# Performance work log

Hardware: AMD Instinct MI355X
Metric: run time of the kernel (lower is better)

## Reference

```python
import jax, jax.numpy as jnp
import numpy as np

BETA = 10.0
EPS = 1e-6


def setup_inputs() -> dict:
    key = jax.random.key(0)
    k0, k1 = jax.random.split(key)
    f0 = jax.random.normal(k0, (4, 256, 64, 64), dtype=jnp.float32)
    f1 = jax.random.normal(k1, (4, 256, 64, 64), dtype=jnp.float32)
    return {"f0": f0, "f1": f1}


def _l2norm(x, axis):
    norm = jnp.sqrt(jnp.sum(x * x, axis=axis, keepdims=True))
    return x / jnp.maximum(norm, EPS)


def reference(f0, f1):
    B, C, Ha, Wa = f0.shape
    _, _, Hb, Wb = f1.shape
    # [B, HaWa, C] and [B, HbWb, C]
    a = f0.reshape(B, C, Ha * Wa).transpose(0, 2, 1)
    b = f1.reshape(B, C, Hb * Wb).transpose(0, 2, 1)
    a = _l2norm(a, axis=2)
    b = _l2norm(b, axis=2)
    # cosine similarity scaled by beta: [B, HaWa, HbWb]
    sim = jnp.einsum('bnc,bmc->bnm', a, b) * BETA
    attn = jax.nn.softmax(sim, axis=2)
    # target coords (x, y) of image1 grid: [HbWb, 2]
    ys = jnp.arange(Hb, dtype=f0.dtype)
    xs = jnp.arange(Wb, dtype=f0.dtype)
    yy, xx = jnp.meshgrid(ys, xs, indexing='ij')
    coords = jnp.stack([xx.reshape(-1), yy.reshape(-1)], axis=1)
    tgt = jnp.einsum('bnm,mk->bnk', attn, coords)
    warp_c = tgt.reshape(B, Ha, Wa, 2)
    cert_c = jnp.max(attn, axis=2).reshape(B, Ha, Wa)
    return (warp_c, cert_c)
```

## Files before the change

kernel.cpp:

```cpp
#include <hip/hip_runtime.h>
#include <hip/hip_bf16.h>

#define BETA_LOG2E 14.426950408889634f
#define EPSN 1e-6f

typedef __bf16 bf16x8 __attribute__((ext_vector_type(8)));
typedef float  f32x4  __attribute__((ext_vector_type(4)));

static __device__ inline unsigned short f2bf(float f) {
    __hip_bfloat16 h = __float2bfloat16(f);
    return __builtin_bit_cast(unsigned short, h);
}
static __device__ inline float bf2f(unsigned short u) {
    unsigned int b = ((unsigned int)u) << 16;
    return __builtin_bit_cast(float, b);
}

__global__ __launch_bounds__(256) void k_norm_transpose(
    const float* __restrict__ f0, const float* __restrict__ f1,
    unsigned short* __restrict__ aT, unsigned short* __restrict__ bT)
{
    __shared__ unsigned short tile[32 * 256];
    __shared__ float partial[32][32];
    __shared__ float inv_l[32];

    int idx   = blockIdx.x;
    int which = idx >> 9;
    int rem   = idx & 511;
    int b     = rem >> 7;
    int n0    = (rem & 127) * 32;
    const float* src = which ? f1 : f0;
    unsigned short* dst = which ? bT : aT;

    int t  = threadIdx.x;
    int nq = t & 7;
    int cg = t >> 3;

    const float* sp = src + ((size_t)(b * 256 + cg * 8)) * 4096 + n0 + nq * 4;

    f32x4 ss = {0.f, 0.f, 0.f, 0.f};
    unsigned int pk[4][4];
#pragma unroll
    for (int i = 0; i < 8; ++i) {
        f32x4 v = *reinterpret_cast<const f32x4*>(sp + (size_t)i * 4096);
        ss += v * v;
#pragma unroll
        for (int j = 0; j < 4; ++j) {
            unsigned int h = f2bf(v[j]);
            if (i & 1) pk[j][i >> 1] |= h << 16;
            else       pk[j][i >> 1]  = h;
        }
    }
#pragma unroll
    for (int j = 0; j < 4; ++j) {
        int n = nq * 4 + j;
        *reinterpret_cast<uint4*>(&tile[n * 256 + cg * 8]) =
            *reinterpret_cast<const uint4*>(pk[j]);
    }
    *reinterpret_cast<f32x4*>(&partial[cg][nq * 4]) = ss;
    __syncthreads();
    if (t < 32) {
        float s = 0.f;
#pragma unroll
        for (int k = 0; k < 32; ++k) s += partial[k][t];
        inv_l[t] = 1.0f / fmaxf(sqrtf(s), EPSN);
    }
    __syncthreads();

#pragma unroll
    for (int it = 0; it < 4; ++it) {
        int n  = it * 8 + (t >> 5);
        int cb = t & 31;
        uint4 v = *reinterpret_cast<const uint4*>(&tile[n * 256 + cb * 8]);
        float inv = inv_l[n];
        unsigned int o[4];
#pragma unroll
        for (int k = 0; k < 4; ++k) {
            unsigned int u = (&v.x)[k];
            unsigned short lo = f2bf(bf2f((unsigned short)(u & 0xffffu)) * inv);
            unsigned short hi = f2bf(bf2f((unsigned short)(u >> 16)) * inv);
            o[k] = (unsigned int)lo | ((unsigned int)hi << 16);
        }
        *reinterpret_cast<uint4*>(&dst[((size_t)(b * 4096 + n0 + n)) * 256 + cb * 8]) =
            *reinterpret_cast<const uint4*>(o);
    }
}

__global__ __launch_bounds__(256) void k_flash(
    const unsigned short* __restrict__ aT, const unsigned short* __restrict__ bT,
    float* __restrict__ stats)
{
    __shared__ unsigned short kb[2 * 64 * 256];

    int idx   = blockIdx.x;
    int xcd   = idx & 7;
    int batch = xcd >> 1;
    int sub   = ((idx >> 3) << 1) | (xcd & 1);
    int qt    = sub >> 2;
    int ks    = sub & 3;

    int t    = threadIdx.x;
    int w    = t >> 6;
    int lane = t & 63;
    int quad = lane >> 4;
    int l15  = lane & 15;
    int q0w  = qt * 128 + w * 32;
    int k0   = ks * 1024;

    bf16x8 afrag[2][8];
#pragma unroll
    for (int s = 0; s < 2; ++s) {
        const unsigned short* ap =
            aT + ((size_t)(batch * 4096 + q0w + s * 16 + l15)) * 256 + quad * 8;
#pragma unroll
        for (int kk = 0; kk < 8; ++kk)
            afrag[s][kk] = *reinterpret_cast<const bf16x8*>(ap + kk * 32);
    }

    int s7 = l15 & 7;
    int offs[8];
#pragma unroll
    for (int kk = 0; kk < 8; ++kk) offs[kk] = (((quad + 4 * kk) ^ s7) << 3);

    int krem = 2 * w + (lane >> 5);
    int goff = krem * 256 + (((lane & 31) ^ (krem & 7)) << 3);

    float Z[8], Sx[8], Sy[8], Pm[8];
#pragma unroll
    for (int i = 0; i < 8; ++i) { Z[i] = 0.f; Sx[i] = 0.f; Sy[i] = 0.f; Pm[i] = 0.f; }

    const unsigned short* gkbase = bT + ((size_t)(batch * 4096 + k0)) * 256;

#define STAGE(CH, BUFHW)                                                        \
    {                                                                           \
        const unsigned short* gsp = gkbase + (size_t)(CH) * 16384 + goff;       \
        unsigned short* lp0 = kb + (BUFHW) + w * 512;                           \
        _Pragma("unroll")                                                       \
        for (int i = 0; i < 8; ++i)                                             \
            __builtin_amdgcn_global_load_lds(                                   \
                (const __attribute__((address_space(1))) void*)(gsp + i * 2048),\
                (__attribute__((address_space(3))) void*)(lp0 + i * 2048),      \
                16, 0, 0);                                                      \
    }

    STAGE(0, 0);
    __syncthreads();
    int bufOff = 0;

    for (int ch = 0; ch < 16; ++ch) {
        if (ch < 15) STAGE(ch + 1, bufOff ^ 16384);

#pragma unroll
        for (int nt = 0; nt < 4; ++nt) {
            f32x4 acc0 = {0.f, 0.f, 0.f, 0.f};
            f32x4 acc1 = {0.f, 0.f, 0.f, 0.f};
            const unsigned short* lp = kb + bufOff + (nt * 16 + l15) * 256;
#pragma unroll
            for (int kk = 0; kk < 8; ++kk) {
                bf16x8 bfrag = *reinterpret_cast<const bf16x8*>(lp + offs[kk]);
                acc0 = __builtin_amdgcn_mfma_f32_16x16x32_bf16(afrag[0][kk], bfrag, acc0, 0, 0, 0);
                acc1 = __builtin_amdgcn_mfma_f32_16x16x32_bf16(afrag[1][kk], bfrag, acc1, 0, 0, 0);
            }
            int key  = k0 + ch * 64 + nt * 16 + l15;
            float kx = (float)(key & 63);
            float ky = (float)(key >> 6);
#pragma unroll
            for (int r = 0; r < 4; ++r) {
                float p0 = exp2f(acc0[r] * BETA_LOG2E);
                Z[r]  += p0;  Sx[r] += p0 * kx;  Sy[r] += p0 * ky;
                Pm[r] = fmaxf(Pm[r], p0);
                float p1 = exp2f(acc1[r] * BETA_LOG2E);
                Z[4 + r]  += p1;  Sx[4 + r] += p1 * kx;  Sy[4 + r] += p1 * ky;
                Pm[4 + r] = fmaxf(Pm[4 + r], p1);
            }
        }
        __syncthreads();
        bufOff ^= 16384;
    }
#undef STAGE

#pragma unroll
    for (int i = 0; i < 8; ++i) {
#pragma unroll
        for (int m = 1; m <= 8; m <<= 1) {
            Z[i]  += __shfl_xor(Z[i], m);
            Sx[i] += __shfl_xor(Sx[i], m);
            Sy[i] += __shfl_xor(Sy[i], m);
            Pm[i]  = fmaxf(Pm[i], __shfl_xor(Pm[i], m));
        }
    }
    if (l15 == 0) {
#pragma unroll
        for (int s = 0; s < 2; ++s)
#pragma unroll
            for (int r = 0; r < 4; ++r) {
                int q = q0w + s * 16 + quad * 4 + r;
                f32x4 st = {Z[s * 4 + r], Sx[s * 4 + r], Sy[s * 4 + r], Pm[s * 4 + r]};
                *reinterpret_cast<f32x4*>(&stats[((size_t)(batch * 4096 + q) * 4 + ks) * 4]) = st;
            }
    }
}

__global__ __launch_bounds__(256) void k_finalize(
    const float* __restrict__ stats, float* __restrict__ out)
{
    int q = blockIdx.x * 256 + threadIdx.x;
    const f32x4* s = reinterpret_cast<const f32x4*>(stats + (size_t)q * 16);
    f32x4 a0 = s[0], a1 = s[1], a2 = s[2], a3 = s[3];
    float Z  = a0.x + a1.x + a2.x + a3.x;
    float Sx = a0.y + a1.y + a2.y + a3.y;
    float Sy = a0.z + a1.z + a2.z + a3.z;
    float Pm = fmaxf(fmaxf(a0.w, a1.w), fmaxf(a2.w, a3.w));
    float invZ = 1.0f / Z;
    out[q * 2 + 0]  = Sx * invZ;
    out[q * 2 + 1]  = Sy * invZ;
    out[32768 + q]  = Pm * invZ;
}

extern "C" void kernel_launch(void* const* d_in, const int* in_sizes, int n_in,
                              void* d_out, int out_size, void* d_ws, size_t ws_size,
                              hipStream_t stream)
{
    const float* f0 = (const float*)d_in[0];
    const float* f1 = (const float*)d_in[1];
    unsigned short* aT = (unsigned short*)d_ws;
    unsigned short* bT = aT + (size_t)4 * 4096 * 256;
    float* stats = (float*)(bT + (size_t)4 * 4096 * 256);
    float* out = (float*)d_out;

    hipLaunchKernelGGL(k_norm_transpose, dim3(1024), dim3(256), 0, stream, f0, f1, aT, bT);
    hipLaunchKernelGGL(k_flash,          dim3(512),  dim3(256), 0, stream, aT, bT, stats);
    hipLaunchKernelGGL(k_finalize,       dim3(64),   dim3(256), 0, stream, stats, out);
}
```

Baseline: 127.1 us.

## Derive y-moment from running prefix sums and track max logit instead of max prob

```diff
diff --git a/kernel.cpp b/kernel.cpp
--- a/kernel.cpp
+++ b/kernel.cpp
@@ -20,28 +20,28 @@
     const float* __restrict__ f0, const float* __restrict__ f1,
     unsigned short* __restrict__ aT, unsigned short* __restrict__ bT)
 {
-    __shared__ unsigned short tile[32 * 256];
-    __shared__ float partial[32][32];
-    __shared__ float inv_l[32];
+    __shared__ unsigned short tile[16 * 256];
+    __shared__ float partial[64][16];
+    __shared__ float inv_l[16];
 
     int idx   = blockIdx.x;
-    int which = idx >> 9;
-    int rem   = idx & 511;
-    int b     = rem >> 7;
-    int n0    = (rem & 127) * 32;
+    int which = idx >> 10;
+    int rem   = idx & 1023;
+    int b     = rem >> 8;
+    int n0    = (rem & 255) * 16;
     const float* src = which ? f1 : f0;
     unsigned short* dst = which ? bT : aT;
 
     int t  = threadIdx.x;
-    int nq = t & 7;
-    int cg = t >> 3;
-
-    const float* sp = src + ((size_t)(b * 256 + cg * 8)) * 4096 + n0 + nq * 4;
+    int nq = t & 3;
+    int cg = t >> 2;
+
+    const float* sp = src + ((size_t)(b * 256 + cg * 4)) * 4096 + n0 + nq * 4;
 
     f32x4 ss = {0.f, 0.f, 0.f, 0.f};
-    unsigned int pk[4][4];
-#pragma unroll
-    for (int i = 0; i < 8; ++i) {
+    unsigned int pk[4][2];
+#pragma unroll
+    for (int i = 0; i < 4; ++i) {
         f32x4 v = *reinterpret_cast<const f32x4*>(sp + (size_t)i * 4096);
         ss += v * v;
 #pragma unroll
@@ -54,35 +54,40 @@
 #pragma unroll
     for (int j = 0; j < 4; ++j) {
         int n = nq * 4 + j;
-        *reinterpret_cast<uint4*>(&tile[n * 256 + cg * 8]) =
-            *reinterpret_cast<const uint4*>(pk[j]);
+        *reinterpret_cast<uint2*>(&tile[n * 256 + cg * 4]) =
+            *reinterpret_cast<const uint2*>(pk[j]);
     }
     *reinterpret_cast<f32x4*>(&partial[cg][nq * 4]) = ss;
     __syncthreads();
-    if (t < 32) {
+    if (t < 16) {
         float s = 0.f;
 #pragma unroll
-        for (int k = 0; k < 32; ++k) s += partial[k][t];
+        for (int k = 0; k < 64; ++k) s += partial[k][t];
         inv_l[t] = 1.0f / fmaxf(sqrtf(s), EPSN);
     }
     __syncthreads();
 
-#pragma unroll
-    for (int it = 0; it < 4; ++it) {
-        int n  = it * 8 + (t >> 5);
-        int cb = t & 31;
-        uint4 v = *reinterpret_cast<const uint4*>(&tile[n * 256 + cb * 8]);
+    {
+        int n  = t >> 4;
+        int c0 = (t & 15) * 16;
         float inv = inv_l[n];
-        unsigned int o[4];
+        uint4 v0 = *reinterpret_cast<const uint4*>(&tile[n * 256 + c0]);
+        uint4 v1 = *reinterpret_cast<const uint4*>(&tile[n * 256 + c0 + 8]);
+        unsigned int o[8];
 #pragma unroll
         for (int k = 0; k < 4; ++k) {
-            unsigned int u = (&v.x)[k];
-            unsigned short lo = f2bf(bf2f((unsigned short)(u & 0xffffu)) * inv);
-            unsigned short hi = f2bf(bf2f((unsigned short)(u >> 16)) * inv);
-            o[k] = (unsigned int)lo | ((unsigned int)hi << 16);
-        }
-        *reinterpret_cast<uint4*>(&dst[((size_t)(b * 4096 + n0 + n)) * 256 + cb * 8]) =
-            *reinterpret_cast<const uint4*>(o);
+            unsigned int u0 = (&v0.x)[k];
+            unsigned int u1 = (&v1.x)[k];
+            unsigned short a0 = f2bf(bf2f((unsigned short)(u0 & 0xffffu)) * inv);
+            unsigned short a1 = f2bf(bf2f((unsigned short)(u0 >> 16)) * inv);
+            unsigned short b0 = f2bf(bf2f((unsigned short)(u1 & 0xffffu)) * inv);
+            unsigned short b1 = f2bf(bf2f((unsigned short)(u1 >> 16)) * inv);
+            o[k]     = (unsigned int)a0 | ((unsigned int)a1 << 16);
+            o[4 + k] = (unsigned int)b0 | ((unsigned int)b1 << 16);
+        }
+        size_t base = ((size_t)(b * 4096 + n0 + n)) * 256 + c0;
+        *reinterpret_cast<uint4*>(&dst[base])     = *reinterpret_cast<const uint4*>(&o[0]);
+        *reinterpret_cast<uint4*>(&dst[base + 8]) = *reinterpret_cast<const uint4*>(&o[4]);
     }
 }
 
@@ -125,9 +130,9 @@
     int krem = 2 * w + (lane >> 5);
     int goff = krem * 256 + (((lane & 31) ^ (krem & 7)) << 3);
 
-    float Z[8], Sx[8], Sy[8], Pm[8];
-#pragma unroll
-    for (int i = 0; i < 8; ++i) { Z[i] = 0.f; Sx[i] = 0.f; Sy[i] = 0.f; Pm[i] = 0.f; }
+    float Z[8], Sx[8], U[8], Sm[8];
+#pragma unroll
+    for (int i = 0; i < 8; ++i) { Z[i] = 0.f; Sx[i] = 0.f; U[i] = 0.f; Sm[i] = -1e30f; }
 
     const unsigned short* gkbase = bT + ((size_t)(batch * 4096 + k0)) * 256;
 
@@ -161,19 +166,19 @@
                 acc0 = __builtin_amdgcn_mfma_f32_16x16x32_bf16(afrag[0][kk], bfrag, acc0, 0, 0, 0);
                 acc1 = __builtin_amdgcn_mfma_f32_16x16x32_bf16(afrag[1][kk], bfrag, acc1, 0, 0, 0);
             }
-            int key  = k0 + ch * 64 + nt * 16 + l15;
-            float kx = (float)(key & 63);
-            float ky = (float)(key >> 6);
+            float kx = (float)(nt * 16 + l15);
 #pragma unroll
             for (int r = 0; r < 4; ++r) {
                 float p0 = exp2f(acc0[r] * BETA_LOG2E);
-                Z[r]  += p0;  Sx[r] += p0 * kx;  Sy[r] += p0 * ky;
-                Pm[r] = fmaxf(Pm[r], p0);
+                Z[r]  += p0;  Sx[r] += p0 * kx;
+                Sm[r]  = fmaxf(Sm[r], acc0[r]);
                 float p1 = exp2f(acc1[r] * BETA_LOG2E);
-                Z[4 + r]  += p1;  Sx[4 + r] += p1 * kx;  Sy[4 + r] += p1 * ky;
-                Pm[4 + r] = fmaxf(Pm[4 + r], p1);
+                Z[4 + r]  += p1;  Sx[4 + r] += p1 * kx;
+                Sm[4 + r]  = fmaxf(Sm[4 + r], acc1[r]);
             }
         }
+#pragma unroll
+        for (int i = 0; i < 8; ++i) U[i] += Z[i];
         __syncthreads();
         bufOff ^= 16384;
     }
@@ -185,17 +190,20 @@
         for (int m = 1; m <= 8; m <<= 1) {
             Z[i]  += __shfl_xor(Z[i], m);
             Sx[i] += __shfl_xor(Sx[i], m);
-            Sy[i] += __shfl_xor(Sy[i], m);
-            Pm[i]  = fmaxf(Pm[i], __shfl_xor(Pm[i], m));
+            U[i]  += __shfl_xor(U[i], m);
+            Sm[i]  = fmaxf(Sm[i], __shfl_xor(Sm[i], m));
         }
     }
     if (l15 == 0) {
+        float kyc = 16.0f * (float)(ks + 1);
 #pragma unroll
         for (int s = 0; s < 2; ++s)
 #pragma unroll
             for (int r = 0; r < 4; ++r) {
                 int q = q0w + s * 16 + quad * 4 + r;
-                f32x4 st = {Z[s * 4 + r], Sx[s * 4 + r], Sy[s * 4 + r], Pm[s * 4 + r]};
+                int i = s * 4 + r;
+                float Sy = kyc * Z[i] - U[i];
+                f32x4 st = {Z[i], Sx[i], Sy, exp2f(Sm[i] * BETA_LOG2E)};
                 *reinterpret_cast<f32x4*>(&stats[((size_t)(batch * 4096 + q) * 4 + ks) * 4]) = st;
             }
     }
@@ -228,7 +236,7 @@
     float* stats = (float*)(bT + (size_t)4 * 4096 * 256);
     float* out = (float*)d_out;
 
-    hipLaunchKernelGGL(k_norm_transpose, dim3(1024), dim3(256), 0, stream, f0, f1, aT, bT);
+    hipLaunchKernelGGL(k_norm_transpose, dim3(2048), dim3(256), 0, stream, f0, f1, aT, bT);
     hipLaunchKernelGGL(k_flash,          dim3(512),  dim3(256), 0, stream, aT, bT, stats);
     hipLaunchKernelGGL(k_finalize,       dim3(64),   dim3(256), 0, stream, stats, out);
 }
```

Result: slower. 131.2 us (+3.2%).

## Fold softmax scale into query normalization and derive coordinate sums from prefix sums

Applied to the files above, without the earlier changes.

```diff
diff --git a/kernel.cpp b/kernel.cpp
--- a/kernel.cpp
+++ b/kernel.cpp
@@ -31,6 +31,7 @@
     int n0    = (rem & 127) * 32;
     const float* src = which ? f1 : f0;
     unsigned short* dst = which ? bT : aT;
+    float scale = which ? 1.0f : BETA_LOG2E;
 
     int t  = threadIdx.x;
     int nq = t & 7;
@@ -63,7 +64,7 @@
         float s = 0.f;
 #pragma unroll
         for (int k = 0; k < 32; ++k) s += partial[k][t];
-        inv_l[t] = 1.0f / fmaxf(sqrtf(s), EPSN);
+        inv_l[t] = scale / fmaxf(sqrtf(s), EPSN);
     }
     __syncthreads();
 
@@ -125,9 +126,9 @@
     int krem = 2 * w + (lane >> 5);
     int goff = krem * 256 + (((lane & 31) ^ (krem & 7)) << 3);
 
-    float Z[8], Sx[8], Sy[8], Pm[8];
-#pragma unroll
-    for (int i = 0; i < 8; ++i) { Z[i] = 0.f; Sx[i] = 0.f; Sy[i] = 0.f; Pm[i] = 0.f; }
+    float Z[8], V[8], U[8], Sm[8];
+#pragma unroll
+    for (int i = 0; i < 8; ++i) { Z[i] = 0.f; V[i] = 0.f; U[i] = 0.f; Sm[i] = -1e30f; }
 
     const unsigned short* gkbase = bT + ((size_t)(batch * 4096 + k0)) * 256;
 
@@ -161,41 +162,52 @@
                 acc0 = __builtin_amdgcn_mfma_f32_16x16x32_bf16(afrag[0][kk], bfrag, acc0, 0, 0, 0);
                 acc1 = __builtin_amdgcn_mfma_f32_16x16x32_bf16(afrag[1][kk], bfrag, acc1, 0, 0, 0);
             }
-            int key  = k0 + ch * 64 + nt * 16 + l15;
-            float kx = (float)(key & 63);
-            float ky = (float)(key >> 6);
 #pragma unroll
             for (int r = 0; r < 4; ++r) {
-                float p0 = exp2f(acc0[r] * BETA_LOG2E);
-                Z[r]  += p0;  Sx[r] += p0 * kx;  Sy[r] += p0 * ky;
-                Pm[r] = fmaxf(Pm[r], p0);
-                float p1 = exp2f(acc1[r] * BETA_LOG2E);
-                Z[4 + r]  += p1;  Sx[4 + r] += p1 * kx;  Sy[4 + r] += p1 * ky;
-                Pm[4 + r] = fmaxf(Pm[4 + r], p1);
-            }
-        }
+                float p0 = exp2f(acc0[r]);
+                Z[r]  += p0;
+                Sm[r]  = fmaxf(Sm[r], acc0[r]);
+                float p1 = exp2f(acc1[r]);
+                Z[4 + r]  += p1;
+                Sm[4 + r]  = fmaxf(Sm[4 + r], acc1[r]);
+            }
+            if (nt < 3) {
+#pragma unroll
+                for (int i = 0; i < 8; ++i) V[i] += Z[i];
+            }
+        }
+#pragma unroll
+        for (int i = 0; i < 8; ++i) U[i] += Z[i];
         __syncthreads();
         bufOff ^= 16384;
     }
 #undef STAGE
 
+    float l15f = (float)l15;
+#pragma unroll
+    for (int i = 0; i < 8; ++i) V[i] = l15f * Z[i] - 16.0f * V[i];
+
 #pragma unroll
     for (int i = 0; i < 8; ++i) {
 #pragma unroll
         for (int m = 1; m <= 8; m <<= 1) {
             Z[i]  += __shfl_xor(Z[i], m);
-            Sx[i] += __shfl_xor(Sx[i], m);
-            Sy[i] += __shfl_xor(Sy[i], m);
-            Pm[i]  = fmaxf(Pm[i], __shfl_xor(Pm[i], m));
+            V[i]  += __shfl_xor(V[i], m);
+            U[i]  += __shfl_xor(U[i], m);
+            Sm[i]  = fmaxf(Sm[i], __shfl_xor(Sm[i], m));
         }
     }
     if (l15 == 0) {
+        float kyc = 16.0f * (float)(ks + 1);
 #pragma unroll
         for (int s = 0; s < 2; ++s)
 #pragma unroll
             for (int r = 0; r < 4; ++r) {
                 int q = q0w + s * 16 + quad * 4 + r;
-                f32x4 st = {Z[s * 4 + r], Sx[s * 4 + r], Sy[s * 4 + r], Pm[s * 4 + r]};
+                int i = s * 4 + r;
+                float Sx = V[i] + 48.0f * U[i];
+                float Sy = kyc * Z[i] - U[i];
+                f32x4 st = {Z[i], Sx, Sy, exp2f(Sm[i])};
                 *reinterpret_cast<f32x4*>(&stats[((size_t)(batch * 4096 + q) * 4 + ks) * 4]) = st;
             }
     }
```

Result: faster. 122.3 us (-3.8%).
